# Optimization experiments

Measured on AMD Instinct MI355X. Metric: run time of the kernel, lower is better.

## Reference

```python
import jax, jax.numpy as jnp
import numpy as np

N = 100000      # nodes
E = 1600000     # edges (avg degree 16)
D_IN, D_H, D_OUT = 128, 128, 64
NORM_SCALE = 1.0
EPS = 1e-6


def setup_inputs() -> dict:
    key = jax.random.key(0)
    ks = jax.random.split(key, 9)
    x = jax.random.normal(ks[0], (N, D_IN), dtype=jnp.float32)
    edge_index = jax.random.randint(ks[1], (2, E), 0, N, dtype=jnp.int32)
    edge_weight = jax.random.uniform(ks[2], (E,), dtype=jnp.float32)
    # GraphConv = Linear then spmm(adj, .); Glorot-ish init for weights
    W0 = jax.random.normal(ks[3], (D_IN, D_H), dtype=jnp.float32) / np.float32(np.sqrt(D_IN))
    b0 = jnp.zeros((D_H,), jnp.float32)
    W1 = jax.random.normal(ks[4], (D_H, D_H), dtype=jnp.float32) / np.float32(np.sqrt(D_H))
    b1 = jnp.zeros((D_H,), jnp.float32)
    Wout = jax.random.normal(ks[5], (D_H, D_OUT), dtype=jnp.float32) / np.float32(np.sqrt(D_H))
    bout = jnp.zeros((D_OUT,), jnp.float32)
    return {"x": x, "edge_index": edge_index, "edge_weight": edge_weight,
            "W0": W0, "b0": b0, "W1": W1, "b1": b1, "Wout": Wout, "bout": bout}


def _pair_norm(h):
    # PairNorm mode 'PN': center columns, divide by sqrt(mean squared row norm)
    h = h - jnp.mean(h, axis=0, keepdims=True)
    rownorm_mean = jnp.sqrt(EPS + jnp.mean(jnp.sum(h * h, axis=1)))
    return NORM_SCALE * h / rownorm_mean


def reference(x, edge_index, edge_weight, W0, b0, W1, b1, Wout, bout):
    src = edge_index[0]
    dst = edge_index[1]

    def graph_conv(h, W, b):
        h = h @ W + b                              # [N, d_out]
        msg = edge_weight[:, None] * h[src]        # [E, d_out] gather
        return jax.ops.segment_sum(msg, dst, num_segments=N)  # spmm(adj, h)

    x_old = jnp.zeros((), jnp.float32)
    for (W, b) in ((W0, b0), (W1, b1)):
        # dropout p=0 -> identity (omitted)
        h = graph_conv(x, W, b)
        h = jax.nn.relu(_pair_norm(h))
        x = h + x_old        # residual=1 -> skip every layer
        x_old = x
    return graph_conv(x, Wout, bout)
```

## Files before the change

kernel.cpp:

```cpp
#include <hip/hip_runtime.h>

#define N_NODES 100000
#define N_EDGES 1600000
#define DH 128
#define DOUT 64
#define EPS 1e-6f
#define NBINS 8
#define BINW 12500
#define NREP 64

typedef __attribute__((ext_vector_type(8))) short s8v;
typedef __attribute__((ext_vector_type(4))) float f32x4;

__device__ inline unsigned bfround(float f) {
    unsigned u = __float_as_uint(f);
    return (u + 0x7fffu + ((u >> 16) & 1u)) >> 16;
}
__device__ inline unsigned pack2(float a, float b) { return bfround(a) | (bfround(b) << 16); }
__device__ inline float blo(unsigned u) { return __uint_as_float(u << 16); }
__device__ inline float bhi(unsigned u) { return __uint_as_float(u & 0xffff0000u); }

template <int COLS, int PN>
__global__ __launch_bounds__(256) void gemm_mfma(const void* __restrict__ Xav,
                                                 const float* __restrict__ cs_partA,
                                                 const float* __restrict__ ss_partA,
                                                 const unsigned* __restrict__ Xbu2,
                                                 const float* __restrict__ cs_partB,
                                                 const float* __restrict__ ss_partB,
                                                 const float* __restrict__ W,
                                                 const float* __restrict__ bias,
                                                 unsigned* __restrict__ Y, int nrows) {
    constexpr int CT = COLS / 16;
    __shared__ unsigned wtu[COLS][64];
    __shared__ unsigned xbu[64][64];
    __shared__ float mulds[2][128];
    __shared__ float invlds[2];
    __shared__ float sstotlds[2];

    const int tid = threadIdx.x;
    const int wv = tid >> 6;
    const int lane = tid & 63;

    {
        ushort* wts = (ushort*)wtu;
        constexpr int NV4 = 128 * COLS / 4;
        for (int i = tid; i < NV4; i += 256) {
            int k = i / (COLS / 4);
            int c4 = i % (COLS / 4);
            float4 w4 = reinterpret_cast<const float4*>(W)[i];
            float vals[4] = {w4.x, w4.y, w4.z, w4.w};
            int u = k >> 1, kb = k & 1;
#pragma unroll
            for (int j = 0; j < 4; ++j) {
                int c = c4 * 4 + j;
                int us = u ^ ((c & 7) << 2);
                wts[c * 128 + us * 2 + kb] = (ushort)bfround(vals[j]);
            }
        }
    }

    if constexpr (PN >= 1) {
        const int set = tid >> 7;
        const int t = tid & 127;
        if (set == 0 || PN == 2) {
            const float* cp = (set == 0) ? cs_partA : cs_partB;
            float m = 0.f;
            for (int r = 0; r < NREP; ++r) m += cp[r * 128 + t];
            mulds[set][t] = m / (float)N_NODES;
        }
        float ssv = 0.f;
        if (wv == 0) ssv = ss_partA[lane];
        else if (PN == 2 && wv == 1) ssv = ss_partB[lane];
#pragma unroll
        for (int off = 32; off; off >>= 1) ssv += __shfl_down(ssv, off, 64);
        if (lane == 0 && wv < 2) sstotlds[wv] = ssv;
        __syncthreads();
        if (wv < ((PN == 2) ? 2 : 1)) {
            float mq = mulds[wv][lane] * mulds[wv][lane] +
                       mulds[wv][lane + 64] * mulds[wv][lane + 64];
#pragma unroll
            for (int off = 32; off; off >>= 1) mq += __shfl_down(mq, off, 64);
            if (lane == 0) {
                float s = (sstotlds[wv] - (float)N_NODES * mq) / (float)N_NODES;
                invlds[wv] = rsqrtf(EPS + s);
            }
        }
        __syncthreads();
    }
    const float sA = (PN >= 1) ? invlds[0] : 0.f;
    const float sB = (PN == 2) ? invlds[1] : 0.f;

    float bv[CT];
#pragma unroll
    for (int f = 0; f < CT; ++f) bv[f] = bias[f * 16 + (lane & 15)];

    const int row0 = blockIdx.x * 128;
    const int myr = (wv << 4) + (lane & 15);

#pragma unroll
    for (int ms = 0; ms < 2; ++ms) {
        const int rb = row0 + ms * 64;
        __syncthreads();
        if constexpr (PN == 0) {
            const float* Xa = (const float*)Xav;
            for (int i = tid; i < 2048; i += 256) {
                int r = i >> 5;
                int c4 = i & 31;
                float4 v = make_float4(0.f, 0.f, 0.f, 0.f);
                if (rb + r < nrows)
                    v = reinterpret_cast<const float4*>(Xa + (size_t)(rb + r) * 128)[c4];
                int sw = (r & 7) << 2;
                xbu[r][(c4 * 2) ^ sw] = pack2(v.x, v.y);
                xbu[r][(c4 * 2 + 1) ^ sw] = pack2(v.z, v.w);
            }
        } else {
            const unsigned* Xa = (const unsigned*)Xav;
            for (int i = tid; i < 1024; i += 256) {
                int r = i >> 4;
                int c4 = i & 15;
                float v0 = 0.f, v1 = 0.f, v2 = 0.f, v3 = 0.f, v4 = 0.f, v5 = 0.f, v6 = 0.f,
                      v7 = 0.f;
                if (rb + r < nrows) {
                    uint4 uv = reinterpret_cast<const uint4*>(Xa + (size_t)(rb + r) * 64)[c4];
                    float4 ma = *reinterpret_cast<const float4*>(&mulds[0][c4 * 8]);
                    float4 mb = *reinterpret_cast<const float4*>(&mulds[0][c4 * 8 + 4]);
                    v0 = fmaxf((blo(uv.x) - ma.x) * sA, 0.f);
                    v1 = fmaxf((bhi(uv.x) - ma.y) * sA, 0.f);
                    v2 = fmaxf((blo(uv.y) - ma.z) * sA, 0.f);
                    v3 = fmaxf((bhi(uv.y) - ma.w) * sA, 0.f);
                    v4 = fmaxf((blo(uv.z) - mb.x) * sA, 0.f);
                    v5 = fmaxf((bhi(uv.z) - mb.y) * sA, 0.f);
                    v6 = fmaxf((blo(uv.w) - mb.z) * sA, 0.f);
                    v7 = fmaxf((bhi(uv.w) - mb.w) * sA, 0.f);
                    if constexpr (PN == 2) {
                        uint4 u2 = reinterpret_cast<const uint4*>(Xbu2 + (size_t)(rb + r) * 64)[c4];
                        float4 na = *reinterpret_cast<const float4*>(&mulds[1][c4 * 8]);
                        float4 nb = *reinterpret_cast<const float4*>(&mulds[1][c4 * 8 + 4]);
                        v0 += fmaxf((blo(u2.x) - na.x) * sB, 0.f);
                        v1 += fmaxf((bhi(u2.x) - na.y) * sB, 0.f);
                        v2 += fmaxf((blo(u2.y) - na.z) * sB, 0.f);
                        v3 += fmaxf((bhi(u2.y) - na.w) * sB, 0.f);
                        v4 += fmaxf((blo(u2.z) - nb.x) * sB, 0.f);
                        v5 += fmaxf((bhi(u2.z) - nb.y) * sB, 0.f);
                        v6 += fmaxf((blo(u2.w) - nb.z) * sB, 0.f);
                        v7 += fmaxf((bhi(u2.w) - nb.w) * sB, 0.f);
                    }
                }
                int sw = (r & 7) << 2;
                xbu[r][(c4 * 4 + 0) ^ sw] = pack2(v0, v1);
                xbu[r][(c4 * 4 + 1) ^ sw] = pack2(v2, v3);
                xbu[r][(c4 * 4 + 2) ^ sw] = pack2(v4, v5);
                xbu[r][(c4 * 4 + 3) ^ sw] = pack2(v6, v7);
            }
        }
        __syncthreads();

        f32x4 acc[CT];
#pragma unroll
        for (int f = 0; f < CT; ++f) acc[f] = (f32x4){0.f, 0.f, 0.f, 0.f};
        const int xsw = (myr & 7) << 2;
#pragma unroll
        for (int kc = 0; kc < 4; ++kc) {
            const int u0 = kc * 16 + (lane >> 4) * 4;
            s8v a = *reinterpret_cast<const s8v*>(&xbu[myr][u0 ^ xsw]);
#pragma unroll
            for (int f = 0; f < CT; ++f) {
                const int c = f * 16 + (lane & 15);
                s8v b = *reinterpret_cast<const s8v*>(&wtu[c][u0 ^ ((c & 7) << 2)]);
                acc[f] = __builtin_amdgcn_mfma_f32_16x16x32_bf16(a, b, acc[f], 0, 0, 0);
            }
        }

#pragma unroll
        for (int f = 0; f < CT; ++f) {
#pragma unroll
            for (int r = 0; r < 4; ++r) {
                float v = acc[f][r] + bv[f];
                float p = __shfl_xor(v, 1, 64);
                unsigned pk = (lane & 1) ? pack2(p, v) : pack2(v, p);
                int grow = rb + (wv << 4) + ((lane >> 4) << 2) + r;
                if (grow < nrows && ((lane & 1) == (f & 1))) {
                    Y[(size_t)grow * (COLS / 2) + f * 8 + ((lane & 15) >> 1)] = pk;
                }
            }
        }
    }
}

__global__ __launch_bounds__(256) void hist_kernel(const int* __restrict__ dst,
                                                   int* __restrict__ counts) {
    int i = blockIdx.x * blockDim.x + threadIdx.x;
    const int stride = gridDim.x * blockDim.x;
    for (; i < N_EDGES / 4; i += stride) {
        int4 d = reinterpret_cast<const int4*>(dst)[i];
        atomicAdd(&counts[d.x], 1);
        atomicAdd(&counts[d.y], 1);
        atomicAdd(&counts[d.z], 1);
        atomicAdd(&counts[d.w], 1);
    }
}

__global__ __launch_bounds__(1024) void scan_kernel(const int* __restrict__ counts,
                                                    int* __restrict__ rowptr) {
    __shared__ int wsum[16];
    const int tid = threadIdx.x;
    const int lane = tid & 63;
    const int w = tid >> 6;
    int offset = 0;
    if (tid == 0) rowptr[0] = 0;
    for (int base = 0; base < N_NODES; base += 4096) {
        int i = base + tid * 4;
        int4 v = make_int4(0, 0, 0, 0);
        if (i < N_NODES) v = *reinterpret_cast<const int4*>(counts + i);
        int p0 = v.x, p1 = p0 + v.y, p2 = p1 + v.z, p3 = p2 + v.w;
        int incl = p3;
#pragma unroll
        for (int d = 1; d < 64; d <<= 1) {
            int t = __shfl_up(incl, d, 64);
            if (lane >= d) incl += t;
        }
        if (lane == 63) wsum[w] = incl;
        __syncthreads();
        if (w == 0 && lane < 16) {
            int t = wsum[lane];
#pragma unroll
            for (int d = 1; d < 16; d <<= 1) {
                int u = __shfl_up(t, d, 64);
                if (lane >= d) t += u;
            }
            wsum[lane] = t;
        }
        __syncthreads();
        int woff = (w == 0) ? 0 : wsum[w - 1];
        int chunk_total = wsum[15];
        int tbase = offset + woff + incl - p3;
        if (i < N_NODES) {
            rowptr[i + 1] = tbase + p0;
            rowptr[i + 2] = tbase + p1;
            rowptr[i + 3] = tbase + p2;
            rowptr[i + 4] = tbase + p3;
        }
        offset += chunk_total;
        __syncthreads();
    }
}

__global__ __launch_bounds__(256) void bucket_kernel(const int* __restrict__ src,
                                                     const int* __restrict__ dst,
                                                     const float* __restrict__ ew,
                                                     const int* __restrict__ rowptr,
                                                     int* __restrict__ fill,
                                                     int2* __restrict__ em) {
    const int myBin = blockIdx.x & (NBINS - 1);
    const int lo = myBin * BINW;
    const int hi = lo + BINW;
    int e = (blockIdx.x >> 3) * 256 + threadIdx.x;
    const int stride = (gridDim.x >> 3) * 256;
    for (; e < N_EDGES; e += stride) {
        int d = dst[e];
        if (d >= lo && d < hi) {
            int pos = atomicAdd(&fill[d], 1);
            em[rowptr[d] + pos] = make_int2(src[e], __float_as_int(ew[e]));
        }
    }
}

__global__ __launch_bounds__(256) void agg128b_kernel(const unsigned* __restrict__ Hb,
                                                      const int* __restrict__ rowptr,
                                                      const int2* __restrict__ em,
                                                      unsigned* __restrict__ Bb,
                                                      float* __restrict__ cs_part,
                                                      float* __restrict__ ss_part) {
    __shared__ int2 smeta[4][64];
    __shared__ float cs[4][128];
    __shared__ float ssw[4];
    const int wv = threadIdx.x >> 6;
    const int lane = threadIdx.x & 63;
    const int half = lane >> 5;
    const int col2 = lane & 31;
    const int node = blockIdx.x * 4 + wv;
    const int beg = rowptr[node];
    const int end = rowptr[node + 1];
    const int2* sm = smeta[wv];
    float a0 = 0.f, a1 = 0.f, a2 = 0.f, a3 = 0.f;

    for (int c = beg; c < end; c += 64) {
        smeta[wv][lane] = (c + lane < end) ? em[c + lane] : make_int2(0, 0);
        const int cnt = min(64, end - c);
        const int rounds = (cnt + 15) >> 4;
        for (int g = 0; g < rounds; ++g) {
            const int b = g * 16 + half;
            int2 m0 = sm[b + 0];
            int2 m1 = sm[b + 2];
            int2 m2 = sm[b + 4];
            int2 m3 = sm[b + 6];
            int2 m4 = sm[b + 8];
            int2 m5 = sm[b + 10];
            int2 m6 = sm[b + 12];
            int2 m7 = sm[b + 14];
            uint2 u0 = *reinterpret_cast<const uint2*>(Hb + (size_t)m0.x * 64 + col2 * 2);
            uint2 u1 = *reinterpret_cast<const uint2*>(Hb + (size_t)m1.x * 64 + col2 * 2);
            uint2 u2 = *reinterpret_cast<const uint2*>(Hb + (size_t)m2.x * 64 + col2 * 2);
            uint2 u3 = *reinterpret_cast<const uint2*>(Hb + (size_t)m3.x * 64 + col2 * 2);
            uint2 u4 = *reinterpret_cast<const uint2*>(Hb + (size_t)m4.x * 64 + col2 * 2);
            uint2 u5 = *reinterpret_cast<const uint2*>(Hb + (size_t)m5.x * 64 + col2 * 2);
            uint2 u6 = *reinterpret_cast<const uint2*>(Hb + (size_t)m6.x * 64 + col2 * 2);
            uint2 u7 = *reinterpret_cast<const uint2*>(Hb + (size_t)m7.x * 64 + col2 * 2);
            float w0 = __int_as_float(m0.y), w1 = __int_as_float(m1.y);
            float w2 = __int_as_float(m2.y), w3 = __int_as_float(m3.y);
            float w4 = __int_as_float(m4.y), w5 = __int_as_float(m5.y);
            float w6 = __int_as_float(m6.y), w7 = __int_as_float(m7.y);
            a0 += w0 * blo(u0.x); a1 += w0 * bhi(u0.x); a2 += w0 * blo(u0.y); a3 += w0 * bhi(u0.y);
            a0 += w1 * blo(u1.x); a1 += w1 * bhi(u1.x); a2 += w1 * blo(u1.y); a3 += w1 * bhi(u1.y);
            a0 += w2 * blo(u2.x); a1 += w2 * bhi(u2.x); a2 += w2 * blo(u2.y); a3 += w2 * bhi(u2.y);
            a0 += w3 * blo(u3.x); a1 += w3 * bhi(u3.x); a2 += w3 * blo(u3.y); a3 += w3 * bhi(u3.y);
            a0 += w4 * blo(u4.x); a1 += w4 * bhi(u4.x); a2 += w4 * blo(u4.y); a3 += w4 * bhi(u4.y);
            a0 += w5 * blo(u5.x); a1 += w5 * bhi(u5.x); a2 += w5 * blo(u5.y); a3 += w5 * bhi(u5.y);
            a0 += w6 * blo(u6.x); a1 += w6 * bhi(u6.x); a2 += w6 * blo(u6.y); a3 += w6 * bhi(u6.y);
            a0 += w7 * blo(u7.x); a1 += w7 * bhi(u7.x); a2 += w7 * blo(u7.y); a3 += w7 * bhi(u7.y);
        }
    }
    a0 += __shfl_xor(a0, 32, 64);
    a1 += __shfl_xor(a1, 32, 64);
    a2 += __shfl_xor(a2, 32, 64);
    a3 += __shfl_xor(a3, 32, 64);

    float sq = 0.f;
    if (lane < 32) {
        uint2 op;
        op.x = pack2(a0, a1);
        op.y = pack2(a2, a3);
        *reinterpret_cast<uint2*>(Bb + (size_t)node * 64 + col2 * 2) = op;
        cs[wv][col2 * 4 + 0] = a0;
        cs[wv][col2 * 4 + 1] = a1;
        cs[wv][col2 * 4 + 2] = a2;
        cs[wv][col2 * 4 + 3] = a3;
        sq = a0 * a0 + a1 * a1 + a2 * a2 + a3 * a3;
    }
#pragma unroll
    for (int off = 32; off; off >>= 1) sq += __shfl_down(sq, off, 64);
    if (lane == 0) ssw[wv] = sq;
    __syncthreads();
    const int rep = blockIdx.x & (NREP - 1);
    if (threadIdx.x < 128) {
        float s = cs[0][threadIdx.x] + cs[1][threadIdx.x] + cs[2][threadIdx.x] + cs[3][threadIdx.x];
        atomicAdd(&cs_part[rep * 128 + threadIdx.x], s);
    }
    if (threadIdx.x == 0) atomicAdd(&ss_part[rep], ssw[0] + ssw[1] + ssw[2] + ssw[3]);
}

__global__ __launch_bounds__(256) void agg64b_kernel(const unsigned* __restrict__ Hb,
                                                     const int* __restrict__ rowptr,
                                                     const int2* __restrict__ em,
                                                     float* __restrict__ out) {
    __shared__ int2 smeta[4][64];
    const int wv = threadIdx.x >> 6;
    const int lane = threadIdx.x & 63;
    const int q = lane >> 4;
    const int col2 = lane & 15;
    const int node = blockIdx.x * 4 + wv;
    const int beg = rowptr[node];
    const int end = rowptr[node + 1];
    const int2* sm = smeta[wv];
    float a0 = 0.f, a1 = 0.f, a2 = 0.f, a3 = 0.f;

    for (int c = beg; c < end; c += 64) {
        smeta[wv][lane] = (c + lane < end) ? em[c + lane] : make_int2(0, 0);
        const int cnt = min(64, end - c);
        const int rounds = (cnt + 31) >> 5;
        for (int g = 0; g < rounds; ++g) {
            const int b = g * 32 + q;
            int2 m0 = sm[b + 0];
            int2 m1 = sm[b + 4];
            int2 m2 = sm[b + 8];
            int2 m3 = sm[b + 12];
            int2 m4 = sm[b + 16];
            int2 m5 = sm[b + 20];
            int2 m6 = sm[b + 24];
            int2 m7 = sm[b + 28];
            uint2 u0 = *reinterpret_cast<const uint2*>(Hb + (size_t)m0.x * 32 + col2 * 2);
            uint2 u1 = *reinterpret_cast<const uint2*>(Hb + (size_t)m1.x * 32 + col2 * 2);
            uint2 u2 = *reinterpret_cast<const uint2*>(Hb + (size_t)m2.x * 32 + col2 * 2);
            uint2 u3 = *reinterpret_cast<const uint2*>(Hb + (size_t)m3.x * 32 + col2 * 2);
            uint2 u4 = *reinterpret_cast<const uint2*>(Hb + (size_t)m4.x * 32 + col2 * 2);
            uint2 u5 = *reinterpret_cast<const uint2*>(Hb + (size_t)m5.x * 32 + col2 * 2);
            uint2 u6 = *reinterpret_cast<const uint2*>(Hb + (size_t)m6.x * 32 + col2 * 2);
            uint2 u7 = *reinterpret_cast<const uint2*>(Hb + (size_t)m7.x * 32 + col2 * 2);
            float w0 = __int_as_float(m0.y), w1 = __int_as_float(m1.y);
            float w2 = __int_as_float(m2.y), w3 = __int_as_float(m3.y);
            float w4 = __int_as_float(m4.y), w5 = __int_as_float(m5.y);
            float w6 = __int_as_float(m6.y), w7 = __int_as_float(m7.y);
            a0 += w0 * blo(u0.x); a1 += w0 * bhi(u0.x); a2 += w0 * blo(u0.y); a3 += w0 * bhi(u0.y);
            a0 += w1 * blo(u1.x); a1 += w1 * bhi(u1.x); a2 += w1 * blo(u1.y); a3 += w1 * bhi(u1.y);
            a0 += w2 * blo(u2.x); a1 += w2 * bhi(u2.x); a2 += w2 * blo(u2.y); a3 += w2 * bhi(u2.y);
            a0 += w3 * blo(u3.x); a1 += w3 * bhi(u3.x); a2 += w3 * blo(u3.y); a3 += w3 * bhi(u3.y);
            a0 += w4 * blo(u4.x); a1 += w4 * bhi(u4.x); a2 += w4 * blo(u4.y); a3 += w4 * bhi(u4.y);
            a0 += w5 * blo(u5.x); a1 += w5 * bhi(u5.x); a2 += w5 * blo(u5.y); a3 += w5 * bhi(u5.y);
            a0 += w6 * blo(u6.x); a1 += w6 * bhi(u6.x); a2 += w6 * blo(u6.y); a3 += w6 * bhi(u6.y);
            a0 += w7 * blo(u7.x); a1 += w7 * bhi(u7.x); a2 += w7 * blo(u7.y); a3 += w7 * bhi(u7.y);
        }
    }
    a0 += __shfl_xor(a0, 16, 64); a0 += __shfl_xor(a0, 32, 64);
    a1 += __shfl_xor(a1, 16, 64); a1 += __shfl_xor(a1, 32, 64);
    a2 += __shfl_xor(a2, 16, 64); a2 += __shfl_xor(a2, 32, 64);
    a3 += __shfl_xor(a3, 16, 64); a3 += __shfl_xor(a3, 32, 64);
    if (lane < 16) {
        *reinterpret_cast<float4*>(out + (size_t)node * DOUT + col2 * 4) =
            make_float4(a0, a1, a2, a3);
    }
}

extern "C" void kernel_launch(void* const* d_in, const int* in_sizes, int n_in,
                              void* d_out, int out_size, void* d_ws, size_t ws_size,
                              hipStream_t stream) {
    const float* x = (const float*)d_in[0];
    const int* edge_index = (const int*)d_in[1];
    const float* ew = (const float*)d_in[2];
    const float* W0 = (const float*)d_in[3];
    const float* b0 = (const float*)d_in[4];
    const float* W1 = (const float*)d_in[5];
    const float* b1 = (const float*)d_in[6];
    const float* Wout = (const float*)d_in[7];
    const float* bout = (const float*)d_in[8];

    const int* src = edge_index;
    const int* dst = edge_index + N_EDGES;
    float* out = (float*)d_out;

    unsigned* base = (unsigned*)d_ws;
    unsigned* Hb = base;
    unsigned* B1b = base + (size_t)N_NODES * 64;
    unsigned* B2b = B1b + (size_t)N_NODES * 64;
    int2* em = (int2*)(B2b + (size_t)N_NODES * 64);
    int* counts = (int*)(em + N_EDGES);
    int* fill = counts + N_NODES;
    int* rowptr = fill + N_NODES;
    size_t soff = (size_t)(rowptr + N_NODES + 1 - (int*)base);
    soff = (soff + 3) & ~(size_t)3;
    float* stats = (float*)base + soff;
    float* cs_part1 = stats;
    float* ss_part1 = cs_part1 + NREP * 128;
    float* cs_part2 = ss_part1 + NREP;
    float* ss_part2 = cs_part2 + NREP * 128;

    const int gemm_grid = (N_NODES + 127) / 128;
    const int agg_grid = N_NODES / 4;

    hipMemsetAsync(counts, 0, (size_t)2 * N_NODES * sizeof(int), stream);
    hipMemsetAsync(stats, 0, (size_t)2 * (NREP * 128 + NREP) * sizeof(float), stream);

    hist_kernel<<<1024, 256, 0, stream>>>(dst, counts);
    scan_kernel<<<1, 1024, 0, stream>>>(counts, rowptr);
    bucket_kernel<<<2048, 256, 0, stream>>>(src, dst, ew, rowptr, fill, em);

    gemm_mfma<128, 0><<<gemm_grid, 256, 0, stream>>>(
        x, nullptr, nullptr, nullptr, nullptr, nullptr, W0, b0, Hb, N_NODES);
    agg128b_kernel<<<agg_grid, 256, 0, stream>>>(Hb, rowptr, em, B1b, cs_part1, ss_part1);

    gemm_mfma<128, 1><<<gemm_grid, 256, 0, stream>>>(
        B1b, cs_part1, ss_part1, nullptr, nullptr, nullptr, W1, b1, Hb, N_NODES);
    agg128b_kernel<<<agg_grid, 256, 0, stream>>>(Hb, rowptr, em, B2b, cs_part2, ss_part2);

    gemm_mfma<64, 2><<<gemm_grid, 256, 0, stream>>>(
        B2b, cs_part2, ss_part2, B1b, cs_part1, ss_part1, Wout, bout, Hb, N_NODES);
    agg64b_kernel<<<agg_grid, 256, 0, stream>>>(Hb, rowptr, em, out);
}
```

Baseline: 542.4 us.

## Store features in column-sliced layout and aggregate per slice for cache locality

Intermediate bf16 feature matrices are stored as 8 column slices of 16 features each (slice-major), written by the GEMM epilogue and read back in the same layout. The aggregation kernels now launch one block per (64-node group, slice), with 4 lanes per node each gathering 8 bytes per edge, so each slice's working set (about 3.2 MB) can stay resident in cache during the random gathers. The trade-off is that edge metadata is re-read once per slice (8x or 4x), each gather is only 32 bytes per node, and the work per node is serial over its edges with less lane parallelism.

```diff
diff --git a/kernel.cpp b/kernel.cpp
--- a/kernel.cpp
+++ b/kernel.cpp
@@ -8,6 +8,7 @@
 #define NBINS 8
 #define BINW 12500
 #define NREP 64
+#define NGRP ((N_NODES + 63) / 64)
 
 typedef __attribute__((ext_vector_type(8))) short s8v;
 typedef __attribute__((ext_vector_type(4))) float f32x4;
@@ -115,13 +116,18 @@
             }
         } else {
             const unsigned* Xa = (const unsigned*)Xav;
-            for (int i = tid; i < 1024; i += 256) {
-                int r = i >> 4;
-                int c4 = i & 15;
+#pragma unroll
+            for (int pass = 0; pass < 4; ++pass) {
+                int s = pass * 2 + (tid >> 7);
+                int t = tid & 127;
+                int r = t >> 1;
+                int half = t & 1;
+                int c4 = s * 2 + half;
                 float v0 = 0.f, v1 = 0.f, v2 = 0.f, v3 = 0.f, v4 = 0.f, v5 = 0.f, v6 = 0.f,
                       v7 = 0.f;
                 if (rb + r < nrows) {
-                    uint4 uv = reinterpret_cast<const uint4*>(Xa + (size_t)(rb + r) * 64)[c4];
+                    uint4 uv = *reinterpret_cast<const uint4*>(
+                        Xa + (size_t)s * ((size_t)N_NODES * 8) + (size_t)(rb + r) * 8 + half * 4);
                     float4 ma = *reinterpret_cast<const float4*>(&mulds[0][c4 * 8]);
                     float4 mb = *reinterpret_cast<const float4*>(&mulds[0][c4 * 8 + 4]);
                     v0 = fmaxf((blo(uv.x) - ma.x) * sA, 0.f);
@@ -133,7 +139,9 @@
                     v6 = fmaxf((blo(uv.w) - mb.z) * sA, 0.f);
                     v7 = fmaxf((bhi(uv.w) - mb.w) * sA, 0.f);
                     if constexpr (PN == 2) {
-                        uint4 u2 = reinterpret_cast<const uint4*>(Xbu2 + (size_t)(rb + r) * 64)[c4];
+                        uint4 u2 = *reinterpret_cast<const uint4*>(
+                            Xbu2 + (size_t)s * ((size_t)N_NODES * 8) + (size_t)(rb + r) * 8 +
+                            half * 4);
                         float4 na = *reinterpret_cast<const float4*>(&mulds[1][c4 * 8]);
                         float4 nb = *reinterpret_cast<const float4*>(&mulds[1][c4 * 8 + 4]);
                         v0 += fmaxf((blo(u2.x) - na.x) * sB, 0.f);
@@ -180,7 +188,8 @@
                 unsigned pk = (lane & 1) ? pack2(p, v) : pack2(v, p);
                 int grow = rb + (wv << 4) + ((lane >> 4) << 2) + r;
                 if (grow < nrows && ((lane & 1) == (f & 1))) {
-                    Y[(size_t)grow * (COLS / 2) + f * 8 + ((lane & 15) >> 1)] = pk;
+                    Y[(size_t)f * ((size_t)N_NODES * 8) + (size_t)grow * 8 + ((lane & 15) >> 1)] =
+                        pk;
                 }
             }
         }
@@ -265,147 +274,137 @@
     }
 }
 
-__global__ __launch_bounds__(256) void agg128b_kernel(const unsigned* __restrict__ Hb,
+__global__ __launch_bounds__(256) void agg128s_kernel(const unsigned* __restrict__ Hs,
                                                       const int* __restrict__ rowptr,
                                                       const int2* __restrict__ em,
-                                                      unsigned* __restrict__ Bb,
+                                                      unsigned* __restrict__ Bs,
                                                       float* __restrict__ cs_part,
                                                       float* __restrict__ ss_part) {
-    __shared__ int2 smeta[4][64];
-    __shared__ float cs[4][128];
-    __shared__ float ssw[4];
+    __shared__ float csl[4][16];
+    __shared__ float ssl4[4];
+    const int slice = blockIdx.x & 7;
+    const int grp = blockIdx.x >> 3;
     const int wv = threadIdx.x >> 6;
     const int lane = threadIdx.x & 63;
-    const int half = lane >> 5;
-    const int col2 = lane & 31;
-    const int node = blockIdx.x * 4 + wv;
-    const int beg = rowptr[node];
-    const int end = rowptr[node + 1];
-    const int2* sm = smeta[wv];
+    const int g = lane >> 2;
+    const int f = lane & 3;
+    const int node = grp * 64 + wv * 16 + g;
+    const unsigned* hsl = Hs + (size_t)slice * ((size_t)N_NODES * 8) + f * 2;
+
+    int beg = 0, end = 0;
+    if (node < N_NODES) {
+        beg = rowptr[node];
+        end = rowptr[node + 1];
+    }
+
     float a0 = 0.f, a1 = 0.f, a2 = 0.f, a3 = 0.f;
-
-    for (int c = beg; c < end; c += 64) {
-        smeta[wv][lane] = (c + lane < end) ? em[c + lane] : make_int2(0, 0);
-        const int cnt = min(64, end - c);
-        const int rounds = (cnt + 15) >> 4;
-        for (int g = 0; g < rounds; ++g) {
-            const int b = g * 16 + half;
-            int2 m0 = sm[b + 0];
-            int2 m1 = sm[b + 2];
-            int2 m2 = sm[b + 4];
-            int2 m3 = sm[b + 6];
-            int2 m4 = sm[b + 8];
-            int2 m5 = sm[b + 10];
-            int2 m6 = sm[b + 12];
-            int2 m7 = sm[b + 14];
-            uint2 u0 = *reinterpret_cast<const uint2*>(Hb + (size_t)m0.x * 64 + col2 * 2);
-            uint2 u1 = *reinterpret_cast<const uint2*>(Hb + (size_t)m1.x * 64 + col2 * 2);
-            uint2 u2 = *reinterpret_cast<const uint2*>(Hb + (size_t)m2.x * 64 + col2 * 2);
-            uint2 u3 = *reinterpret_cast<const uint2*>(Hb + (size_t)m3.x * 64 + col2 * 2);
-            uint2 u4 = *reinterpret_cast<const uint2*>(Hb + (size_t)m4.x * 64 + col2 * 2);
-            uint2 u5 = *reinterpret_cast<const uint2*>(Hb + (size_t)m5.x * 64 + col2 * 2);
-            uint2 u6 = *reinterpret_cast<const uint2*>(Hb + (size_t)m6.x * 64 + col2 * 2);
-            uint2 u7 = *reinterpret_cast<const uint2*>(Hb + (size_t)m7.x * 64 + col2 * 2);
-            float w0 = __int_as_float(m0.y), w1 = __int_as_float(m1.y);
-            float w2 = __int_as_float(m2.y), w3 = __int_as_float(m3.y);
-            float w4 = __int_as_float(m4.y), w5 = __int_as_float(m5.y);
-            float w6 = __int_as_float(m6.y), w7 = __int_as_float(m7.y);
-            a0 += w0 * blo(u0.x); a1 += w0 * bhi(u0.x); a2 += w0 * blo(u0.y); a3 += w0 * bhi(u0.y);
-            a0 += w1 * blo(u1.x); a1 += w1 * bhi(u1.x); a2 += w1 * blo(u1.y); a3 += w1 * bhi(u1.y);
-            a0 += w2 * blo(u2.x); a1 += w2 * bhi(u2.x); a2 += w2 * blo(u2.y); a3 += w2 * bhi(u2.y);
-            a0 += w3 * blo(u3.x); a1 += w3 * bhi(u3.x); a2 += w3 * blo(u3.y); a3 += w3 * bhi(u3.y);
-            a0 += w4 * blo(u4.x); a1 += w4 * bhi(u4.x); a2 += w4 * blo(u4.y); a3 += w4 * bhi(u4.y);
-            a0 += w5 * blo(u5.x); a1 += w5 * bhi(u5.x); a2 += w5 * blo(u5.y); a3 += w5 * bhi(u5.y);
-            a0 += w6 * blo(u6.x); a1 += w6 * bhi(u6.x); a2 += w6 * blo(u6.y); a3 += w6 * bhi(u6.y);
-            a0 += w7 * blo(u7.x); a1 += w7 * bhi(u7.x); a2 += w7 * blo(u7.y); a3 += w7 * bhi(u7.y);
-        }
-    }
-    a0 += __shfl_xor(a0, 32, 64);
-    a1 += __shfl_xor(a1, 32, 64);
-    a2 += __shfl_xor(a2, 32, 64);
-    a3 += __shfl_xor(a3, 32, 64);
-
-    float sq = 0.f;
-    if (lane < 32) {
+    int e = beg;
+    for (; e + 4 <= end; e += 4) {
+        int2 m0 = em[e];
+        int2 m1 = em[e + 1];
+        int2 m2 = em[e + 2];
+        int2 m3 = em[e + 3];
+        uint2 u0 = *reinterpret_cast<const uint2*>(hsl + (size_t)m0.x * 8);
+        uint2 u1 = *reinterpret_cast<const uint2*>(hsl + (size_t)m1.x * 8);
+        uint2 u2 = *reinterpret_cast<const uint2*>(hsl + (size_t)m2.x * 8);
+        uint2 u3 = *reinterpret_cast<const uint2*>(hsl + (size_t)m3.x * 8);
+        float w0 = __int_as_float(m0.y), w1 = __int_as_float(m1.y);
+        float w2 = __int_as_float(m2.y), w3 = __int_as_float(m3.y);
+        a0 += w0 * blo(u0.x); a1 += w0 * bhi(u0.x); a2 += w0 * blo(u0.y); a3 += w0 * bhi(u0.y);
+        a0 += w1 * blo(u1.x); a1 += w1 * bhi(u1.x); a2 += w1 * blo(u1.y); a3 += w1 * bhi(u1.y);
+        a0 += w2 * blo(u2.x); a1 += w2 * bhi(u2.x); a2 += w2 * blo(u2.y); a3 += w2 * bhi(u2.y);
+        a0 += w3 * blo(u3.x); a1 += w3 * bhi(u3.x); a2 += w3 * blo(u3.y); a3 += w3 * bhi(u3.y);
+    }
+    for (; e < end; ++e) {
+        int2 m = em[e];
+        uint2 u = *reinterpret_cast<const uint2*>(hsl + (size_t)m.x * 8);
+        float w = __int_as_float(m.y);
+        a0 += w * blo(u.x); a1 += w * bhi(u.x); a2 += w * blo(u.y); a3 += w * bhi(u.y);
+    }
+
+    if (node < N_NODES) {
         uint2 op;
         op.x = pack2(a0, a1);
         op.y = pack2(a2, a3);
-        *reinterpret_cast<uint2*>(Bb + (size_t)node * 64 + col2 * 2) = op;
-        cs[wv][col2 * 4 + 0] = a0;
-        cs[wv][col2 * 4 + 1] = a1;
-        cs[wv][col2 * 4 + 2] = a2;
-        cs[wv][col2 * 4 + 3] = a3;
-        sq = a0 * a0 + a1 * a1 + a2 * a2 + a3 * a3;
-    }
-#pragma unroll
-    for (int off = 32; off; off >>= 1) sq += __shfl_down(sq, off, 64);
-    if (lane == 0) ssw[wv] = sq;
+        *reinterpret_cast<uint2*>(Bs + (size_t)slice * ((size_t)N_NODES * 8) + (size_t)node * 8 +
+                                  f * 2) = op;
+    }
+
+    float c0 = a0, c1 = a1, c2 = a2, c3 = a3;
+    float sq = a0 * a0 + a1 * a1 + a2 * a2 + a3 * a3;
+#pragma unroll
+    for (int off = 4; off <= 32; off <<= 1) {
+        c0 += __shfl_xor(c0, off, 64);
+        c1 += __shfl_xor(c1, off, 64);
+        c2 += __shfl_xor(c2, off, 64);
+        c3 += __shfl_xor(c3, off, 64);
+        sq += __shfl_xor(sq, off, 64);
+    }
+    sq += __shfl_xor(sq, 1, 64);
+    sq += __shfl_xor(sq, 2, 64);
+    if (lane < 4) {
+        csl[wv][f * 4 + 0] = c0;
+        csl[wv][f * 4 + 1] = c1;
+        csl[wv][f * 4 + 2] = c2;
+        csl[wv][f * 4 + 3] = c3;
+    }
+    if (lane == 0) ssl4[wv] = sq;
     __syncthreads();
-    const int rep = blockIdx.x & (NREP - 1);
-    if (threadIdx.x < 128) {
-        float s = cs[0][threadIdx.x] + cs[1][threadIdx.x] + cs[2][threadIdx.x] + cs[3][threadIdx.x];
-        atomicAdd(&cs_part[rep * 128 + threadIdx.x], s);
-    }
-    if (threadIdx.x == 0) atomicAdd(&ss_part[rep], ssw[0] + ssw[1] + ssw[2] + ssw[3]);
-}
-
-__global__ __launch_bounds__(256) void agg64b_kernel(const unsigned* __restrict__ Hb,
+    const int rep = grp & (NREP - 1);
+    if (threadIdx.x < 16) {
+        float s = csl[0][threadIdx.x] + csl[1][threadIdx.x] + csl[2][threadIdx.x] +
+                  csl[3][threadIdx.x];
+        atomicAdd(&cs_part[rep * 128 + slice * 16 + threadIdx.x], s);
+    }
+    if (threadIdx.x == 0) atomicAdd(&ss_part[rep], ssl4[0] + ssl4[1] + ssl4[2] + ssl4[3]);
+}
+
+__global__ __launch_bounds__(256) void agg64s_kernel(const unsigned* __restrict__ Hs,
                                                      const int* __restrict__ rowptr,
                                                      const int2* __restrict__ em,
                                                      float* __restrict__ out) {
-    __shared__ int2 smeta[4][64];
+    const int slice = blockIdx.x & 3;
+    const int grp = blockIdx.x >> 2;
     const int wv = threadIdx.x >> 6;
     const int lane = threadIdx.x & 63;
-    const int q = lane >> 4;
-    const int col2 = lane & 15;
-    const int node = blockIdx.x * 4 + wv;
-    const int beg = rowptr[node];
-    const int end = rowptr[node + 1];
-    const int2* sm = smeta[wv];
+    const int g = lane >> 2;
+    const int f = lane & 3;
+    const int node = grp * 64 + wv * 16 + g;
+    const unsigned* hsl = Hs + (size_t)slice * ((size_t)N_NODES * 8) + f * 2;
+
+    int beg = 0, end = 0;
+    if (node < N_NODES) {
+        beg = rowptr[node];
+        end = rowptr[node + 1];
+    }
+
     float a0 = 0.f, a1 = 0.f, a2 = 0.f, a3 = 0.f;
-
-    for (int c = beg; c < end; c += 64) {
-        smeta[wv][lane] = (c + lane < end) ? em[c + lane] : make_int2(0, 0);
-        const int cnt = min(64, end - c);
-        const int rounds = (cnt + 31) >> 5;
-        for (int g = 0; g < rounds; ++g) {
-            const int b = g * 32 + q;
-            int2 m0 = sm[b + 0];
-            int2 m1 = sm[b + 4];
-            int2 m2 = sm[b + 8];
-            int2 m3 = sm[b + 12];
-            int2 m4 = sm[b + 16];
-            int2 m5 = sm[b + 20];
-            int2 m6 = sm[b + 24];
-            int2 m7 = sm[b + 28];
-            uint2 u0 = *reinterpret_cast<const uint2*>(Hb + (size_t)m0.x * 32 + col2 * 2);
-            uint2 u1 = *reinterpret_cast<const uint2*>(Hb + (size_t)m1.x * 32 + col2 * 2);
-            uint2 u2 = *reinterpret_cast<const uint2*>(Hb + (size_t)m2.x * 32 + col2 * 2);
-            uint2 u3 = *reinterpret_cast<const uint2*>(Hb + (size_t)m3.x * 32 + col2 * 2);
-            uint2 u4 = *reinterpret_cast<const uint2*>(Hb + (size_t)m4.x * 32 + col2 * 2);
-            uint2 u5 = *reinterpret_cast<const uint2*>(Hb + (size_t)m5.x * 32 + col2 * 2);
-            uint2 u6 = *reinterpret_cast<const uint2*>(Hb + (size_t)m6.x * 32 + col2 * 2);
-            uint2 u7 = *reinterpret_cast<const uint2*>(Hb + (size_t)m7.x * 32 + col2 * 2);
-            float w0 = __int_as_float(m0.y), w1 = __int_as_float(m1.y);
-            float w2 = __int_as_float(m2.y), w3 = __int_as_float(m3.y);
-            float w4 = __int_as_float(m4.y), w5 = __int_as_float(m5.y);
-            float w6 = __int_as_float(m6.y), w7 = __int_as_float(m7.y);
-            a0 += w0 * blo(u0.x); a1 += w0 * bhi(u0.x); a2 += w0 * blo(u0.y); a3 += w0 * bhi(u0.y);
-            a0 += w1 * blo(u1.x); a1 += w1 * bhi(u1.x); a2 += w1 * blo(u1.y); a3 += w1 * bhi(u1.y);
-            a0 += w2 * blo(u2.x); a1 += w2 * bhi(u2.x); a2 += w2 * blo(u2.y); a3 += w2 * bhi(u2.y);
-            a0 += w3 * blo(u3.x); a1 += w3 * bhi(u3.x); a2 += w3 * blo(u3.y); a3 += w3 * bhi(u3.y);
-            a0 += w4 * blo(u4.x); a1 += w4 * bhi(u4.x); a2 += w4 * blo(u4.y); a3 += w4 * bhi(u4.y);
-            a0 += w5 * blo(u5.x); a1 += w5 * bhi(u5.x); a2 += w5 * blo(u5.y); a3 += w5 * bhi(u5.y);
-            a0 += w6 * blo(u6.x); a1 += w6 * bhi(u6.x); a2 += w6 * blo(u6.y); a3 += w6 * bhi(u6.y);
-            a0 += w7 * blo(u7.x); a1 += w7 * bhi(u7.x); a2 += w7 * blo(u7.y); a3 += w7 * bhi(u7.y);
-        }
-    }
-    a0 += __shfl_xor(a0, 16, 64); a0 += __shfl_xor(a0, 32, 64);
-    a1 += __shfl_xor(a1, 16, 64); a1 += __shfl_xor(a1, 32, 64);
-    a2 += __shfl_xor(a2, 16, 64); a2 += __shfl_xor(a2, 32, 64);
-    a3 += __shfl_xor(a3, 16, 64); a3 += __shfl_xor(a3, 32, 64);
-    if (lane < 16) {
-        *reinterpret_cast<float4*>(out + (size_t)node * DOUT + col2 * 4) =
+    int e = beg;
+    for (; e + 4 <= end; e += 4) {
+        int2 m0 = em[e];
+        int2 m1 = em[e + 1];
+        int2 m2 = em[e + 2];
+        int2 m3 = em[e + 3];
+        uint2 u0 = *reinterpret_cast<const uint2*>(hsl + (size_t)m0.x * 8);
+        uint2 u1 = *reinterpret_cast<const uint2*>(hsl + (size_t)m1.x * 8);
+        uint2 u2 = *reinterpret_cast<const uint2*>(hsl + (size_t)m2.x * 8);
+        uint2 u3 = *reinterpret_cast<const uint2*>(hsl + (size_t)m3.x * 8);
+        float w0 = __int_as_float(m0.y), w1 = __int_as_float(m1.y);
+        float w2 = __int_as_float(m2.y), w3 = __int_as_float(m3.y);
+        a0 += w0 * blo(u0.x); a1 += w0 * bhi(u0.x); a2 += w0 * blo(u0.y); a3 += w0 * bhi(u0.y);
+        a0 += w1 * blo(u1.x); a1 += w1 * bhi(u1.x); a2 += w1 * blo(u1.y); a3 += w1 * bhi(u1.y);
+        a0 += w2 * blo(u2.x); a1 += w2 * bhi(u2.x); a2 += w2 * blo(u2.y); a3 += w2 * bhi(u2.y);
+        a0 += w3 * blo(u3.x); a1 += w3 * bhi(u3.x); a2 += w3 * blo(u3.y); a3 += w3 * bhi(u3.y);
+    }
+    for (; e < end; ++e) {
+        int2 m = em[e];
+        uint2 u = *reinterpret_cast<const uint2*>(hsl + (size_t)m.x * 8);
+        float w = __int_as_float(m.y);
+        a0 += w * blo(u.x); a1 += w * bhi(u.x); a2 += w * blo(u.y); a3 += w * bhi(u.y);
+    }
+
+    if (node < N_NODES) {
+        *reinterpret_cast<float4*>(out + (size_t)node * DOUT + slice * 16 + f * 4) =
             make_float4(a0, a1, a2, a3);
     }
 }
@@ -444,7 +443,8 @@
     float* ss_part2 = cs_part2 + NREP * 128;
 
     const int gemm_grid = (N_NODES + 127) / 128;
-    const int agg_grid = N_NODES / 4;
+    const int agg128_grid = NGRP * 8;
+    const int agg64_grid = NGRP * 4;
 
     hipMemsetAsync(counts, 0, (size_t)2 * N_NODES * sizeof(int), stream);
     hipMemsetAsync(stats, 0, (size_t)2 * (NREP * 128 + NREP) * sizeof(float), stream);
@@ -455,13 +455,13 @@
 
     gemm_mfma<128, 0><<<gemm_grid, 256, 0, stream>>>(
         x, nullptr, nullptr, nullptr, nullptr, nullptr, W0, b0, Hb, N_NODES);
-    agg128b_kernel<<<agg_grid, 256, 0, stream>>>(Hb, rowptr, em, B1b, cs_part1, ss_part1);
+    agg128s_kernel<<<agg128_grid, 256, 0, stream>>>(Hb, rowptr, em, B1b, cs_part1, ss_part1);
 
     gemm_mfma<128, 1><<<gemm_grid, 256, 0, stream>>>(
         B1b, cs_part1, ss_part1, nullptr, nullptr, nullptr, W1, b1, Hb, N_NODES);
-    agg128b_kernel<<<agg_grid, 256, 0, stream>>>(Hb, rowptr, em, B2b, cs_part2, ss_part2);
+    agg128s_kernel<<<agg128_grid, 256, 0, stream>>>(Hb, rowptr, em, B2b, cs_part2, ss_part2);
 
     gemm_mfma<64, 2><<<gemm_grid, 256, 0, stream>>>(
         B2b, cs_part2, ss_part2, B1b, cs_part1, ss_part1, Wout, bout, Hb, N_NODES);
-    agg64b_kernel<<<agg_grid, 256, 0, stream>>>(Hb, rowptr, em, out);
-}
+    agg64s_kernel<<<agg64_grid, 256, 0, stream>>>(Hb, rowptr, em, out);
+}
```

After: 541.2 us. About the same (-0.2%).
